# Performance work log

Hardware: AMD Instinct MI355X
Metric: run time of the kernel (lower is better)

The kernel has to match this reference:

```python
import jax, jax.numpy as jnp
import numpy as np
import math

NUM_HEADS = 16
KEY_SIZE = 64
HIDDEN = 4096
EMBED = 1024
VOCAB = 32000
SEQ = 2048
LAYERS = 4


def rmsnorm(x):
    return x * jax.lax.rsqrt(jnp.mean(x * x, axis=-1, keepdims=True) + 1e-5)


def rope_buffers(seq, d):
    half = d // 2
    i = jnp.arange(d)
    offset = i % half
    scales = jnp.power(10000.0, (-2.0 / d) * offset.astype(jnp.float32))
    m = jnp.arange(seq, dtype=jnp.float32)
    angles = m[:, None] * scales[None, :]  # [S, D]
    cos = jnp.cos(angles)
    sin = jnp.sin(angles)
    sin = jnp.concatenate([-sin[:, :half], sin[:, half:]], axis=-1)
    return cos, sin


def rotate(x, cos, sin):
    # x: [B, H, S, D]; cos/sin: [S, D]
    half = KEY_SIZE // 2
    swapped = jnp.concatenate([x[..., half:], x[..., :half]], axis=-1)
    return cos[None, None] * x + sin[None, None] * swapped


def setup_inputs() -> dict:
    key = jax.random.key(0)
    ks = jax.random.split(key, 7)
    std = 0.02
    return {
        'tokens': jax.random.randint(ks[0], (1, SEQ), 0, VOCAB),
        'table': jax.random.normal(ks[1], (VOCAB, EMBED), jnp.float32) * std,
        'qkv_w': jax.random.normal(ks[2], (LAYERS, EMBED, 3 * NUM_HEADS * KEY_SIZE), jnp.float32) * std,
        'out_w': jax.random.normal(ks[3], (LAYERS, NUM_HEADS * KEY_SIZE, EMBED), jnp.float32) * std,
        'up_w': jax.random.normal(ks[4], (LAYERS, EMBED, 2 * HIDDEN), jnp.float32) * std,
        'down_w': jax.random.normal(ks[5], (LAYERS, HIDDEN, EMBED), jnp.float32) * std,
        'vocab_w': jax.random.normal(ks[6], (EMBED, VOCAB), jnp.float32) * std,
    }


def reference(tokens, table, qkv_w, out_w, up_w, down_w, vocab_w):
    B, S = tokens.shape
    H, D = NUM_HEADS, KEY_SIZE
    # module zeroes embedding row 0 each forward
    table = table.at[0].set(0.0)
    cos, sin = rope_buffers(S, D)
    causal = jnp.tril(jnp.ones((S, S), dtype=bool))  # context_size == S -> pure causal
    emb = table[tokens]  # [B, S, E]
    for l in range(LAYERS):
        # --- self attention ---
        normed = rmsnorm(emb)
        qkv = normed @ qkv_w[l]  # [B, S, 3HD]
        q, k, v = jnp.split(qkv, 3, axis=-1)
        q = q.reshape(B, S, H, D).transpose(0, 2, 1, 3)
        k = k.reshape(B, S, H, D).transpose(0, 2, 1, 3)
        v = v.reshape(B, S, H, D).transpose(0, 2, 1, 3)
        q = rotate(q, cos, sin)
        k = rotate(k, cos, sin)
        attn = jnp.einsum('bhqd,bhkd->bhqk', q, k) / math.sqrt(D)
        attn = jnp.where(causal[None, None], attn, -jnp.inf)
        attn = jax.nn.softmax(attn, axis=-1)
        out = jnp.einsum('bhqk,bhkd->bhqd', attn, v)
        out = out.transpose(0, 2, 1, 3).reshape(B, S, H * D)
        emb = emb + out @ out_w[l]
        # --- SwiGLU FFN ---
        normed = rmsnorm(emb)
        gate_up = normed @ up_w[l]
        gate, up = gate_up[..., :HIDDEN], gate_up[..., HIDDEN:]
        emb = emb + (up * jax.nn.silu(gate)) @ down_w[l]
    emb = rmsnorm(emb)
    logits = emb @ vocab_w  # [B, S, V]
    return logits
```

## Files before the change

### kernel.cpp

```cpp
#include <hip/hip_runtime.h>
#include <hip/hip_bf16.h>

typedef __attribute__((ext_vector_type(8))) short short8;
typedef __attribute__((ext_vector_type(4))) float f32x4;

__device__ __forceinline__ ushort f2bf(float f) {
  uint32_t u = __float_as_uint(f);
  uint32_t r = (u + 0x7FFFu + ((u >> 16) & 1u)) >> 16;
  return (ushort)r;
}
__device__ __forceinline__ float bf2f(ushort u) {
  return __uint_as_float(((uint32_t)u) << 16);
}

__device__ __forceinline__ void gload_lds16(const ushort* g, ushort* l) {
  __builtin_amdgcn_global_load_lds(
      (const __attribute__((address_space(1))) void*)g,
      (__attribute__((address_space(3))) void*)l, 16, 0, 0);
}

__device__ __forceinline__ f32x4 mfma16(short8 a, short8 b, f32x4 c) {
  return __builtin_amdgcn_mfma_f32_16x16x32_bf16(a, b, c, 0, 0, 0);
}

#define BAR() __builtin_amdgcn_s_barrier()
#define WAIT_LGKM()                                        \
  do {                                                     \
    asm volatile("s_waitcnt lgkmcnt(0)" ::: "memory");     \
    __builtin_amdgcn_sched_barrier(0);                     \
  } while (0)
#define WAIT_VM()                                          \
  do {                                                     \
    asm volatile("s_waitcnt vmcnt(0)" ::: "memory");       \
    __builtin_amdgcn_sched_barrier(0);                     \
  } while (0)

__global__ __launch_bounds__(256)
void transpose_conv_kernel(const float* __restrict__ W, ushort* __restrict__ WT,
                           const int K, const int N) {
  __shared__ float tile[32][33];
  const int n0 = blockIdx.x * 32;
  const int k0 = blockIdx.y * 32;
  const int x = threadIdx.x;
  const int y = threadIdx.y;
#pragma unroll
  for (int j = 0; j < 4; ++j)
    tile[y + j * 8][x] = W[(size_t)(k0 + y + j * 8) * N + n0 + x];
  __syncthreads();
#pragma unroll
  for (int j = 0; j < 4; ++j)
    WT[(size_t)(n0 + y + j * 8) * K + k0 + x] = f2bf(tile[x][y + j * 8]);
}

__global__ __launch_bounds__(256)
void embed_kernel(const int* __restrict__ tokens, const float* __restrict__ table,
                  float* __restrict__ emb) {
  const int s = blockIdx.x, t = threadIdx.x;
  const int tok = tokens[s];
  float4 v = make_float4(0.f, 0.f, 0.f, 0.f);
  if (tok != 0) v = *(const float4*)&table[(size_t)tok * 1024 + t * 4];
  *(float4*)&emb[(size_t)s * 1024 + t * 4] = v;
}

__global__ __launch_bounds__(256)
void rmsnorm_kernel(const float* __restrict__ x, ushort* __restrict__ out) {
  const int row = blockIdx.x, t = threadIdx.x;
  const float4 v = *(const float4*)&x[(size_t)row * 1024 + t * 4];
  float ss = v.x * v.x + v.y * v.y + v.z * v.z + v.w * v.w;
#pragma unroll
  for (int off = 32; off; off >>= 1) ss += __shfl_xor(ss, off);
  __shared__ float red[4];
  if ((t & 63) == 0) red[t >> 6] = ss;
  __syncthreads();
  const float total = red[0] + red[1] + red[2] + red[3];
  const float sc = rsqrtf(total * (1.f / 1024.f) + 1e-5f);
  ushort4 o;
  o.x = f2bf(v.x * sc); o.y = f2bf(v.y * sc);
  o.z = f2bf(v.z * sc); o.w = f2bf(v.w * sc);
  *(ushort4*)&out[(size_t)row * 1024 + t * 4] = o;
}

__global__ __launch_bounds__(256)
void rope_kernel(const float* __restrict__ qkv, ushort* __restrict__ qh,
                 ushort* __restrict__ kh) {
  const int s = blockIdx.x;
  const int t = threadIdx.x;
  const int e0 = t * 4;
  const int hh = e0 >> 6;
  const int d0 = e0 & 63;
  const float* row = qkv + (size_t)s * 3072;
  const int part = hh * 64 + ((d0 + 32) & 63);
  const float4 xq  = *(const float4*)&row[e0];
  const float4 xqs = *(const float4*)&row[part];
  const float4 xk  = *(const float4*)&row[1024 + e0];
  const float4 xks = *(const float4*)&row[1024 + part];
  float co[4], si[4];
#pragma unroll
  for (int c = 0; c < 4; ++c) {
    const int d = d0 + c;
    const int off = d & 31;
    const float freq = exp2f(-0.41524101186092029f * (float)off);
    const float ang = (float)s * freq;
    co[c] = cosf(ang);
    const float sv = sinf(ang);
    si[c] = (d < 32) ? -sv : sv;
  }
  ushort4 oq, ok;
  oq.x = f2bf(co[0] * xq.x + si[0] * xqs.x);
  oq.y = f2bf(co[1] * xq.y + si[1] * xqs.y);
  oq.z = f2bf(co[2] * xq.z + si[2] * xqs.z);
  oq.w = f2bf(co[3] * xq.w + si[3] * xqs.w);
  ok.x = f2bf(co[0] * xk.x + si[0] * xks.x);
  ok.y = f2bf(co[1] * xk.y + si[1] * xks.y);
  ok.z = f2bf(co[2] * xk.z + si[2] * xks.z);
  ok.w = f2bf(co[3] * xk.w + si[3] * xks.w);
  const size_t ho = ((size_t)hh * 2048 + s) * 64 + d0;
  *(ushort4*)&qh[ho] = oq;
  *(ushort4*)&kh[ho] = ok;
}

__global__ __launch_bounds__(256)
void vtrans_kernel(const float* __restrict__ qkvbuf, ushort* __restrict__ vt) {
  __shared__ float t[64][65];
  const int h = blockIdx.y;
  const int s0 = blockIdx.x * 64;
  const int tid = threadIdx.x;
#pragma unroll
  for (int j = 0; j < 4; ++j) {
    const int e = j * 1024 + tid * 4;
    const int r = e >> 6, c = e & 63;
    *(float4*)&t[r][c] = *(const float4*)&qkvbuf[(size_t)(s0 + r) * 3072 + 2048 + h * 64 + c];
  }
  __syncthreads();
#pragma unroll
  for (int j = 0; j < 4; ++j) {
    const int e = j * 1024 + tid * 4;
    const int d = e >> 6, s = e & 63;
    ushort4 ov;
    ov.x = f2bf(t[s + 0][d]);
    ov.y = f2bf(t[s + 1][d]);
    ov.z = f2bf(t[s + 2][d]);
    ov.w = f2bf(t[s + 3][d]);
    *(ushort4*)&vt[((size_t)h * 64 + d) * 2048 + s0 + s] = ov;
  }
}

__global__ __launch_bounds__(256)
void attn_mfma_kernel(const ushort* __restrict__ qh, const ushort* __restrict__ kh,
                      const ushort* __restrict__ vt, ushort* __restrict__ attn_out) {
  __shared__ ushort sQ[64 * 64];
  __shared__ ushort sK[64 * 64];
  __shared__ ushort sV[64 * 64];
  __shared__ ushort sP[4][1024];
  const int h = blockIdx.y;
  const int bx = blockIdx.x;
  const int qt = (h < 8) ? bx : 31 - bx;
  const int i0 = qt * 64;
  const int tid = threadIdx.x;
  const int w = tid >> 6, lane = tid & 63;
  const int llo = lane & 15, lhi = lane >> 4;
  const int lr = lane >> 3, lc = lane & 7;
  const ushort* qg = qh + ((size_t)h * 2048 + i0) * 64;
  const ushort* kg = kh + (size_t)h * 2048 * 64;
  const ushort* vg = vt + (size_t)h * 64 * 2048;

#pragma unroll
  for (int j = 0; j < 2; ++j) {
    const int r0 = (w * 2 + j) * 8;
    const int row = r0 + lr;
    gload_lds16(qg + (size_t)row * 64 + ((lc ^ (row & 7)) * 8), &sQ[r0 * 64]);
  }
  __syncthreads();
  const int qrow = w * 16 + llo;
  const short8 qf0 = *(const short8*)&sQ[qrow * 64 + ((lhi ^ (qrow & 7)) * 8)];
  const short8 qf1 = *(const short8*)&sQ[qrow * 64 + (((4 + lhi) ^ (qrow & 7)) * 8)];

  float m = -1e30f, lsum = 0.f;
  f32x4 o[4] = {};
  const int nch = qt + 1;
  for (int cb = 0; cb < nch; ++cb) {
    const int kb = cb * 64;
    __syncthreads();
#pragma unroll
    for (int j = 0; j < 2; ++j) {
      const int r0 = (w * 2 + j) * 8;
      const int row = r0 + lr;
      gload_lds16(kg + (size_t)(kb + row) * 64 + ((lc ^ (row & 7)) * 8), &sK[r0 * 64]);
      gload_lds16(vg + (size_t)row * 2048 + kb + ((lc ^ (row & 7)) * 8), &sV[r0 * 64]);
    }
    __syncthreads();

    f32x4 st[4] = {};
#pragma unroll
    for (int ck = 0; ck < 2; ++ck) {
      const short8 qf = ck ? qf1 : qf0;
#pragma unroll
      for (int f = 0; f < 4; ++f) {
        const int key = f * 16 + llo;
        const short8 kf = *(const short8*)&sK[key * 64 + (((ck * 4 + lhi) ^ (key & 7)) * 8)];
        st[f] = mfma16(kf, qf, st[f]);
      }
    }

    float pv[4][4];
    const bool diag = (kb == i0);
#pragma unroll
    for (int f = 0; f < 4; ++f)
#pragma unroll
      for (int r = 0; r < 4; ++r) {
        float x = st[f][r] * 0.125f;
        if (diag && (f * 16 + lhi * 4 + r) > qrow) x = -1e30f;
        pv[f][r] = x;
      }
    float mr = pv[0][0];
#pragma unroll
    for (int f = 0; f < 4; ++f)
#pragma unroll
      for (int r = 0; r < 4; ++r) mr = fmaxf(mr, pv[f][r]);
    mr = fmaxf(mr, __shfl_xor(mr, 16));
    mr = fmaxf(mr, __shfl_xor(mr, 32));
    const float mnew = fmaxf(m, mr);
    const float scale = __expf(m - mnew);
    m = mnew;
    float rs = 0.f;
#pragma unroll
    for (int f = 0; f < 4; ++f)
#pragma unroll
      for (int r = 0; r < 4; ++r) {
        const float p = __expf(pv[f][r] - mnew);
        pv[f][r] = p;
        rs += p;
      }
    rs += __shfl_xor(rs, 16);
    rs += __shfl_xor(rs, 32);
    lsum = lsum * scale + rs;
    float scr[4];
#pragma unroll
    for (int r = 0; r < 4; ++r) scr[r] = __shfl(scale, lhi * 4 + r);
#pragma unroll
    for (int nn = 0; nn < 4; ++nn)
#pragma unroll
      for (int r = 0; r < 4; ++r) o[nn][r] *= scr[r];

    ushort* pw = sP[w];
#pragma unroll
    for (int f = 0; f < 4; ++f) {
      uint2 pk;
      pk.x = (uint)f2bf(pv[f][0]) | ((uint)f2bf(pv[f][1]) << 16);
      pk.y = (uint)f2bf(pv[f][2]) | ((uint)f2bf(pv[f][3]) << 16);
      *(uint2*)&pw[llo * 64 + ((f * 16 + lhi * 4) ^ ((llo & 7) << 3))] = pk;
    }
    const short8 pf0 = *(const short8*)&pw[llo * 64 + ((lhi ^ (llo & 7)) * 8)];
    const short8 pf1 = *(const short8*)&pw[llo * 64 + (((4 + lhi) ^ (llo & 7)) * 8)];

#pragma unroll
    for (int ck = 0; ck < 2; ++ck) {
      const short8 pf = ck ? pf1 : pf0;
#pragma unroll
      for (int nn = 0; nn < 4; ++nn) {
        const int drow = nn * 16 + llo;
        const short8 vf = *(const short8*)&sV[drow * 64 + (((ck * 4 + lhi) ^ (drow & 7)) * 8)];
        o[nn] = mfma16(pf, vf, o[nn]);
      }
    }
  }

  const float inv = 1.f / lsum;
  float invr[4];
#pragma unroll
  for (int r = 0; r < 4; ++r) invr[r] = __shfl(inv, lhi * 4 + r);
#pragma unroll
  for (int nn = 0; nn < 4; ++nn)
#pragma unroll
    for (int r = 0; r < 4; ++r) {
      const int row = i0 + w * 16 + lhi * 4 + r;
      attn_out[(size_t)row * 1024 + h * 64 + nn * 16 + llo] = f2bf(o[nn][r] * invr[r]);
    }
}

__global__ __launch_bounds__(256)
void silu_mul_kernel(const ushort* __restrict__ gu, ushort* __restrict__ hb) {
  const int idx = blockIdx.x * 256 + threadIdx.x;
  const int i = idx * 4;
  const int r = i >> 12;
  const int c = i & 4095;
  const ushort4 g4 = *(const ushort4*)&gu[(size_t)r * 8192 + c];
  const ushort4 u4 = *(const ushort4*)&gu[(size_t)r * 8192 + 4096 + c];
  ushort4 o;
  {
    float gv = bf2f(g4.x), uv = bf2f(u4.x);
    o.x = f2bf(uv * gv / (1.f + expf(-gv)));
  }
  {
    float gv = bf2f(g4.y), uv = bf2f(u4.y);
    o.y = f2bf(uv * gv / (1.f + expf(-gv)));
  }
  {
    float gv = bf2f(g4.z), uv = bf2f(u4.z);
    o.z = f2bf(uv * gv / (1.f + expf(-gv)));
  }
  {
    float gv = bf2f(g4.w), uv = bf2f(u4.w);
    o.w = f2bf(uv * gv / (1.f + expf(-gv)));
  }
  *(ushort4*)&hb[(size_t)r * 4096 + c] = o;
}

template <int BM, int BN, int EPI>
__global__ __launch_bounds__(256)
void gemm_bt_kernel(const ushort* __restrict__ A, const ushort* __restrict__ BT,
                    const float* __restrict__ addend, void* __restrict__ Cout,
                    const int M, const int N, const int K) {
  constexpr int WM = BM / 2, WN = BN / 2;
  constexpr int FM = WM / 16, FN = WN / 16;
  constexpr int CHA = BM / 16, CHB = BN / 16;
  __shared__ ushort sA[BM * 32];
  __shared__ ushort sB[BN * 32];
  const int bm0 = blockIdx.y * BM;
  const int bn0 = blockIdx.x * BN;
  const int tid = threadIdx.x;
  const int wid = tid >> 6;
  const int lane = tid & 63;
  const int wr = wid >> 1, wc = wid & 1;
  const int lhi = lane >> 4, llo = lane & 15;
  f32x4 acc[FM][FN] = {};
  for (int kt = 0; kt < K; kt += 32) {
#pragma unroll
    for (int c2 = 0; c2 < CHA / 4; ++c2) {
      const int ch = c2 * 4 + wid;
      const int e = ch * 512 + lane * 8;
      gload_lds16(A + (size_t)(bm0 + (e >> 5)) * K + kt + (e & 31), sA + ch * 512);
    }
#pragma unroll
    for (int c2 = 0; c2 < CHB / 4; ++c2) {
      const int ch = c2 * 4 + wid;
      const int e = ch * 512 + lane * 8;
      gload_lds16(BT + (size_t)(bn0 + (e >> 5)) * K + kt + (e & 31), sB + ch * 512);
    }
    __syncthreads();
    short8 aF[FM], bF[FN];
#pragma unroll
    for (int mm = 0; mm < FM; ++mm)
      aF[mm] = *(const short8*)&sA[(wr * WM + mm * 16 + llo) * 32 + lhi * 8];
#pragma unroll
    for (int nn = 0; nn < FN; ++nn)
      bF[nn] = *(const short8*)&sB[(wc * WN + nn * 16 + llo) * 32 + lhi * 8];
#pragma unroll
    for (int mm = 0; mm < FM; ++mm)
#pragma unroll
      for (int nn = 0; nn < FN; ++nn)
        acc[mm][nn] = __builtin_amdgcn_mfma_f32_16x16x32_bf16(aF[mm], bF[nn],
                                                              acc[mm][nn], 0, 0, 0);
    __syncthreads();
  }
#pragma unroll
  for (int mm = 0; mm < FM; ++mm) {
#pragma unroll
    for (int nn = 0; nn < FN; ++nn) {
      const int col = bn0 + wc * WN + nn * 16 + llo;
#pragma unroll
      for (int r = 0; r < 4; ++r) {
        const int row = bm0 + wr * WM + mm * 16 + lhi * 4 + r;
        float v = acc[mm][nn][r];
        if constexpr (EPI == 2) {
          ((ushort*)Cout)[(size_t)row * N + col] = f2bf(v);
        } else {
          if constexpr (EPI == 1) v += addend[(size_t)row * N + col];
          ((float*)Cout)[(size_t)row * N + col] = v;
        }
      }
    }
  }
}

#define LDA_(MH)                                                              \
  {                                                                           \
    _Pragma("unroll") for (int mm = 0; mm < 4; ++mm) {                        \
      const int row = wr * 128 + ((MH) * 4 + mm) * 16 + llo;                  \
      _Pragma("unroll") for (int ks = 0; ks < 2; ++ks)                        \
          aF[mm][ks] = *(const short8*)&cA[row * 64 +                         \
                          (((ks * 4 + lhi) ^ (row & 7)) * 8)];                \
    }                                                                         \
  }
#define LDB_(NH)                                                              \
  {                                                                           \
    _Pragma("unroll") for (int nn = 0; nn < 2; ++nn) {                        \
      const int row = wc * 64 + ((NH) * 2 + nn) * 16 + llo;                   \
      _Pragma("unroll") for (int ks = 0; ks < 2; ++ks)                        \
          bF[nn][ks] = *(const short8*)&cB[row * 64 +                         \
                          (((ks * 4 + lhi) ^ (row & 7)) * 8)];                \
    }                                                                         \
  }
#define MFMAQ_(MH, NH)                                                        \
  {                                                                           \
    __builtin_amdgcn_s_setprio(1);                                            \
    _Pragma("unroll") for (int mm = 0; mm < 4; ++mm)                          \
        _Pragma("unroll") for (int nn = 0; nn < 2; ++nn)                      \
            _Pragma("unroll") for (int ks = 0; ks < 2; ++ks)                  \
                acc[(MH) * 4 + mm][(NH) * 2 + nn] =                           \
                    mfma16(aF[mm][ks], bF[nn][ks],                            \
                           acc[(MH) * 4 + mm][(NH) * 2 + nn]);                \
    __builtin_amdgcn_s_setprio(0);                                            \
  }

template <int EPI>
__global__ __launch_bounds__(512, 2)
void gemm8_kernel(const ushort* __restrict__ A, const ushort* __restrict__ BT,
                  const float* __restrict__ addend, void* __restrict__ Cout,
                  const int M, const int N, const int K, const int nbx) {
  extern __shared__ ushort smem[];
  const int nwg = gridDim.x;
  const int cpx = nwg >> 3;
  int id = blockIdx.x;
  id = (id & 7) * cpx + (id >> 3);
  const int bx = id % nbx, by = id / nbx;
  const int bm0 = by * 256, bn0 = bx * 256;
  const int tid = threadIdx.x;
  const int wid = tid >> 6, lane = tid & 63;
  const int wr = wid >> 2, wc = wid & 3;
  const int llo = lane & 15, lhi = lane >> 4;
  const ushort* gA = A + (size_t)bm0 * K;
  const ushort* gB = BT + (size_t)bn0 * K;

  auto stage = [&](const ushort* g, ushort* dst, int kt) {
#pragma unroll
    for (int i = 0; i < 4; ++i) {
      const int chunk = i * 512 + wid * 64 + lane;
      const int row = chunk >> 3, c = chunk & 7;
      gload_lds16(g + (size_t)row * K + kt + ((c ^ (row & 7)) * 8),
                  dst + (size_t)(i * 512 + wid * 64) * 8);
    }
  };

  f32x4 acc[8][4] = {};
  short8 aF[4][2];
  short8 bF[2][2];

  stage(gA, smem, 0);
  stage(gB, smem + 16384, 0);
  WAIT_VM();
  BAR();

  const int nt = K >> 6;
  for (int t = 0; t < nt; ++t) {
    const int cur = t & 1;
    ushort* cA = smem + cur * 32768;
    ushort* cB = cA + 16384;
    ushort* nA = smem + (cur ^ 1) * 32768;
    ushort* nB = nA + 16384;
    const bool pf = (t + 1 < nt);
    LDA_(0); LDB_(0);
    if (pf) { stage(gA, nA, (t + 1) * 64); stage(gB, nB, (t + 1) * 64); }
    BAR(); WAIT_LGKM();
    MFMAQ_(0, 0);
    BAR();
    LDB_(1);
    BAR(); WAIT_LGKM();
    MFMAQ_(0, 1);
    BAR();
    LDA_(1);
    BAR(); WAIT_LGKM();
    MFMAQ_(1, 1);
    BAR();
    LDB_(0);
    BAR(); WAIT_LGKM();
    MFMAQ_(1, 0);
    if (pf) WAIT_VM();
    BAR();
  }

#pragma unroll
  for (int m = 0; m < 8; ++m) {
#pragma unroll
    for (int n = 0; n < 4; ++n) {
      const int col = bn0 + wc * 64 + n * 16 + llo;
#pragma unroll
      for (int r = 0; r < 4; ++r) {
        const int row = bm0 + wr * 128 + m * 16 + lhi * 4 + r;
        float v = acc[m][n][r];
        if constexpr (EPI == 2) {
          ((ushort*)Cout)[(size_t)row * N + col] = f2bf(v);
        } else {
          if constexpr (EPI == 1) v += addend[(size_t)row * N + col];
          ((float*)Cout)[(size_t)row * N + col] = v;
        }
      }
    }
  }
}

extern "C" void kernel_launch(void* const* d_in, const int* in_sizes, int n_in,
                              void* d_out, int out_size, void* d_ws, size_t ws_size,
                              hipStream_t stream) {
  const int* tokens    = (const int*)d_in[0];
  const float* table   = (const float*)d_in[1];
  const float* qkv_w   = (const float*)d_in[2];
  const float* out_w   = (const float*)d_in[3];
  const float* up_w    = (const float*)d_in[4];
  const float* down_w  = (const float*)d_in[5];
  const float* vocab_w = (const float*)d_in[6];
  float* logits = (float*)d_out;

  constexpr int G8_LDS = 131072;
  hipFuncSetAttribute(reinterpret_cast<const void*>(&gemm8_kernel<0>),
                      hipFuncAttributeMaxDynamicSharedMemorySize, G8_LDS);
  hipFuncSetAttribute(reinterpret_cast<const void*>(&gemm8_kernel<2>),
                      hipFuncAttributeMaxDynamicSharedMemorySize, G8_LDS);

  char* p = (char*)d_ws;
  auto alloc = [&](size_t bytes) {
    char* r = p;
    p += (bytes + 255) & ~(size_t)255;
    return r;
  };
  float*  emb    = (float*)alloc(2048ull * 1024 * 4);
  ushort* normed = (ushort*)alloc(2048ull * 1024 * 2);
  float*  qkvbuf = (float*)alloc(2048ull * 3072 * 4);
  ushort* qhb    = (ushort*)alloc(16ull * 2048 * 64 * 2);
  ushort* khb    = (ushort*)alloc(16ull * 2048 * 64 * 2);
  ushort* vtb    = (ushort*)alloc(16ull * 64 * 2048 * 2);
  ushort* attno  = (ushort*)alloc(2048ull * 1024 * 2);
  ushort* gateup = (ushort*)alloc(2048ull * 8192 * 2);
  ushort* hbuf   = (ushort*)alloc(2048ull * 4096 * 2);
  ushort* qkvT   = (ushort*)alloc(4ull * 3072 * 1024 * 2);
  ushort* outT   = (ushort*)alloc(4ull * 1024 * 1024 * 2);
  ushort* upT    = (ushort*)alloc(4ull * 8192 * 1024 * 2);
  ushort* downT  = (ushort*)alloc(4ull * 1024 * 4096 * 2);
  ushort* vocabT = (ushort*)alloc(32000ull * 1024 * 2);

  const dim3 tb(32, 8);
  for (int l = 0; l < 4; ++l) {
    transpose_conv_kernel<<<dim3(3072 / 32, 1024 / 32), tb, 0, stream>>>(
        qkv_w + (size_t)l * 1024 * 3072, qkvT + (size_t)l * 3072 * 1024, 1024, 3072);
    transpose_conv_kernel<<<dim3(1024 / 32, 1024 / 32), tb, 0, stream>>>(
        out_w + (size_t)l * 1024 * 1024, outT + (size_t)l * 1024 * 1024, 1024, 1024);
    transpose_conv_kernel<<<dim3(8192 / 32, 1024 / 32), tb, 0, stream>>>(
        up_w + (size_t)l * 1024 * 8192, upT + (size_t)l * 8192 * 1024, 1024, 8192);
    transpose_conv_kernel<<<dim3(1024 / 32, 4096 / 32), tb, 0, stream>>>(
        down_w + (size_t)l * 4096 * 1024, downT + (size_t)l * 1024 * 4096, 4096, 1024);
  }
  transpose_conv_kernel<<<dim3(32000 / 32, 1024 / 32), tb, 0, stream>>>(
      vocab_w, vocabT, 1024, 32000);

  embed_kernel<<<2048, 256, 0, stream>>>(tokens, table, emb);

  for (int l = 0; l < 4; ++l) {
    rmsnorm_kernel<<<2048, 256, 0, stream>>>(emb, normed);
    gemm8_kernel<0><<<(3072 / 256) * (2048 / 256), 512, G8_LDS, stream>>>(
        normed, qkvT + (size_t)l * 3072 * 1024, nullptr, qkvbuf,
        2048, 3072, 1024, 3072 / 256);
    rope_kernel<<<2048, 256, 0, stream>>>(qkvbuf, qhb, khb);
    vtrans_kernel<<<dim3(32, 16), 256, 0, stream>>>(qkvbuf, vtb);
    attn_mfma_kernel<<<dim3(32, 16), 256, 0, stream>>>(qhb, khb, vtb, attno);
    gemm_bt_kernel<64, 128, 1><<<dim3(1024 / 128, 2048 / 64), 256, 0, stream>>>(
        attno, outT + (size_t)l * 1024 * 1024, emb, emb, 2048, 1024, 1024);
    rmsnorm_kernel<<<2048, 256, 0, stream>>>(emb, normed);
    gemm8_kernel<2><<<(8192 / 256) * (2048 / 256), 512, G8_LDS, stream>>>(
        normed, upT + (size_t)l * 8192 * 1024, nullptr, gateup,
        2048, 8192, 1024, 8192 / 256);
    silu_mul_kernel<<<8192, 256, 0, stream>>>(gateup, hbuf);
    gemm_bt_kernel<64, 128, 1><<<dim3(1024 / 128, 2048 / 64), 256, 0, stream>>>(
        hbuf, downT + (size_t)l * 1024 * 4096, emb, emb, 2048, 1024, 4096);
  }
  rmsnorm_kernel<<<2048, 256, 0, stream>>>(emb, normed);
  gemm8_kernel<0><<<(32000 / 256) * (2048 / 256), 512, G8_LDS, stream>>>(
      normed, vocabT, nullptr, logits, 2048, 32000, 1024, 32000 / 256);
}
```

Measured before the change: 1.384 ms.

## Fuse SiLU into up-proj GEMM, merge rope/vtrans, retile residual GEMMs

The up-projection weight rows are interleaved so gate and up columns land in adjacent lanes. SwiGLU is then computed in the gemm8 epilogue with a shuffle, which removes the gateup buffer and the separate silu kernel. The rope and V-transpose kernels are merged into one launch, the residual GEMMs move from 64x128 to 128x128 tiles, and the vocab logits use nontemporal stores. The cost is a shuffle-based epilogue in which half the lanes store, and fewer blocks for the residual GEMMs.

```diff
diff --git a/kernel.cpp b/kernel.cpp
--- a/kernel.cpp
+++ b/kernel.cpp
@@ -37,7 +37,7 @@
 
 __global__ __launch_bounds__(256)
 void transpose_conv_kernel(const float* __restrict__ W, ushort* __restrict__ WT,
-                           const int K, const int N) {
+                           const int K, const int N, const int mode) {
   __shared__ float tile[32][33];
   const int n0 = blockIdx.x * 32;
   const int k0 = blockIdx.y * 32;
@@ -48,8 +48,11 @@
     tile[y + j * 8][x] = W[(size_t)(k0 + y + j * 8) * N + n0 + x];
   __syncthreads();
 #pragma unroll
-  for (int j = 0; j < 4; ++j)
-    WT[(size_t)(n0 + y + j * 8) * K + k0 + x] = f2bf(tile[x][y + j * 8]);
+  for (int j = 0; j < 4; ++j) {
+    int r = n0 + y + j * 8;
+    if (mode == 1) r = (r < 4096) ? (2 * r) : (2 * (r - 4096) + 1);
+    WT[(size_t)r * K + k0 + x] = f2bf(tile[x][y + j * 8]);
+  }
 }
 
 __global__ __launch_bounds__(256)
@@ -81,67 +84,59 @@
 }
 
 __global__ __launch_bounds__(256)
-void rope_kernel(const float* __restrict__ qkv, ushort* __restrict__ qh,
-                 ushort* __restrict__ kh) {
-  const int s = blockIdx.x;
-  const int t = threadIdx.x;
-  const int e0 = t * 4;
-  const int hh = e0 >> 6;
-  const int d0 = e0 & 63;
-  const float* row = qkv + (size_t)s * 3072;
-  const int part = hh * 64 + ((d0 + 32) & 63);
-  const float4 xq  = *(const float4*)&row[e0];
-  const float4 xqs = *(const float4*)&row[part];
-  const float4 xk  = *(const float4*)&row[1024 + e0];
-  const float4 xks = *(const float4*)&row[1024 + part];
-  float co[4], si[4];
-#pragma unroll
-  for (int c = 0; c < 4; ++c) {
-    const int d = d0 + c;
-    const int off = d & 31;
-    const float freq = exp2f(-0.41524101186092029f * (float)off);
-    const float ang = (float)s * freq;
-    co[c] = cosf(ang);
-    const float sv = sinf(ang);
-    si[c] = (d < 32) ? -sv : sv;
-  }
-  ushort4 oq, ok;
-  oq.x = f2bf(co[0] * xq.x + si[0] * xqs.x);
-  oq.y = f2bf(co[1] * xq.y + si[1] * xqs.y);
-  oq.z = f2bf(co[2] * xq.z + si[2] * xqs.z);
-  oq.w = f2bf(co[3] * xq.w + si[3] * xqs.w);
-  ok.x = f2bf(co[0] * xk.x + si[0] * xks.x);
-  ok.y = f2bf(co[1] * xk.y + si[1] * xks.y);
-  ok.z = f2bf(co[2] * xk.z + si[2] * xks.z);
-  ok.w = f2bf(co[3] * xk.w + si[3] * xks.w);
-  const size_t ho = ((size_t)hh * 2048 + s) * 64 + d0;
-  *(ushort4*)&qh[ho] = oq;
-  *(ushort4*)&kh[ho] = ok;
-}
-
-__global__ __launch_bounds__(256)
-void vtrans_kernel(const float* __restrict__ qkvbuf, ushort* __restrict__ vt) {
-  __shared__ float t[64][65];
+void ropev_kernel(const float* __restrict__ qkv, ushort* __restrict__ qh,
+                  ushort* __restrict__ kh, ushort* __restrict__ vt) {
+  __shared__ float tv[64][65];
   const int h = blockIdx.y;
   const int s0 = blockIdx.x * 64;
-  const int tid = threadIdx.x;
+  const int t = threadIdx.x;
 #pragma unroll
   for (int j = 0; j < 4; ++j) {
-    const int e = j * 1024 + tid * 4;
-    const int r = e >> 6, c = e & 63;
-    *(float4*)&t[r][c] = *(const float4*)&qkvbuf[(size_t)(s0 + r) * 3072 + 2048 + h * 64 + c];
+    const int e = j * 1024 + t * 4;
+    const int sl = e >> 6, d0 = e & 63;
+    const int s = s0 + sl;
+    const float* row = qkv + (size_t)s * 3072 + h * 64;
+    const float4 xq  = *(const float4*)&row[d0];
+    const float4 xqs = *(const float4*)&row[(d0 + 32) & 63];
+    const float4 xk  = *(const float4*)&row[1024 + d0];
+    const float4 xks = *(const float4*)&row[1024 + ((d0 + 32) & 63)];
+    const float4 xv  = *(const float4*)&row[2048 + d0];
+    float co[4], si[4];
+#pragma unroll
+    for (int c = 0; c < 4; ++c) {
+      const int d = d0 + c;
+      const int off = d & 31;
+      const float freq = exp2f(-0.41524101186092029f * (float)off);
+      const float ang = (float)s * freq;
+      co[c] = cosf(ang);
+      const float sv = sinf(ang);
+      si[c] = (d < 32) ? -sv : sv;
+    }
+    ushort4 oq, ok;
+    oq.x = f2bf(co[0] * xq.x + si[0] * xqs.x);
+    oq.y = f2bf(co[1] * xq.y + si[1] * xqs.y);
+    oq.z = f2bf(co[2] * xq.z + si[2] * xqs.z);
+    oq.w = f2bf(co[3] * xq.w + si[3] * xqs.w);
+    ok.x = f2bf(co[0] * xk.x + si[0] * xks.x);
+    ok.y = f2bf(co[1] * xk.y + si[1] * xks.y);
+    ok.z = f2bf(co[2] * xk.z + si[2] * xks.z);
+    ok.w = f2bf(co[3] * xk.w + si[3] * xks.w);
+    const size_t ho = ((size_t)h * 2048 + s) * 64 + d0;
+    *(ushort4*)&qh[ho] = oq;
+    *(ushort4*)&kh[ho] = ok;
+    *(float4*)&tv[sl][d0] = xv;
   }
   __syncthreads();
 #pragma unroll
   for (int j = 0; j < 4; ++j) {
-    const int e = j * 1024 + tid * 4;
-    const int d = e >> 6, s = e & 63;
+    const int e = j * 1024 + t * 4;
+    const int d = e >> 6, s4 = e & 63;
     ushort4 ov;
-    ov.x = f2bf(t[s + 0][d]);
-    ov.y = f2bf(t[s + 1][d]);
-    ov.z = f2bf(t[s + 2][d]);
-    ov.w = f2bf(t[s + 3][d]);
-    *(ushort4*)&vt[((size_t)h * 64 + d) * 2048 + s0 + s] = ov;
+    ov.x = f2bf(tv[s4 + 0][d]);
+    ov.y = f2bf(tv[s4 + 1][d]);
+    ov.z = f2bf(tv[s4 + 2][d]);
+    ov.w = f2bf(tv[s4 + 3][d]);
+    *(ushort4*)&vt[((size_t)h * 64 + d) * 2048 + s0 + s4] = ov;
   }
 }
 
@@ -276,34 +271,6 @@
       const int row = i0 + w * 16 + lhi * 4 + r;
       attn_out[(size_t)row * 1024 + h * 64 + nn * 16 + llo] = f2bf(o[nn][r] * invr[r]);
     }
-}
-
-__global__ __launch_bounds__(256)
-void silu_mul_kernel(const ushort* __restrict__ gu, ushort* __restrict__ hb) {
-  const int idx = blockIdx.x * 256 + threadIdx.x;
-  const int i = idx * 4;
-  const int r = i >> 12;
-  const int c = i & 4095;
-  const ushort4 g4 = *(const ushort4*)&gu[(size_t)r * 8192 + c];
-  const ushort4 u4 = *(const ushort4*)&gu[(size_t)r * 8192 + 4096 + c];
-  ushort4 o;
-  {
-    float gv = bf2f(g4.x), uv = bf2f(u4.x);
-    o.x = f2bf(uv * gv / (1.f + expf(-gv)));
-  }
-  {
-    float gv = bf2f(g4.y), uv = bf2f(u4.y);
-    o.y = f2bf(uv * gv / (1.f + expf(-gv)));
-  }
-  {
-    float gv = bf2f(g4.z), uv = bf2f(u4.z);
-    o.z = f2bf(uv * gv / (1.f + expf(-gv)));
-  }
-  {
-    float gv = bf2f(g4.w), uv = bf2f(u4.w);
-    o.w = f2bf(uv * gv / (1.f + expf(-gv)));
-  }
-  *(ushort4*)&hb[(size_t)r * 4096 + c] = o;
 }
 
 template <int BM, int BN, int EPI>
@@ -478,10 +445,16 @@
       for (int r = 0; r < 4; ++r) {
         const int row = bm0 + wr * 128 + m * 16 + lhi * 4 + r;
         float v = acc[m][n][r];
-        if constexpr (EPI == 2) {
-          ((ushort*)Cout)[(size_t)row * N + col] = f2bf(v);
+        if constexpr (EPI == 3) {
+          const float other = __shfl_xor(v, 1);
+          if ((llo & 1) == 0) {
+            const float gate = v, up = other;
+            const float hh = up * gate / (1.f + expf(-gate));
+            ((ushort*)Cout)[(size_t)row * (N >> 1) + (col >> 1)] = f2bf(hh);
+          }
+        } else if constexpr (EPI == 4) {
+          __builtin_nontemporal_store(v, &((float*)Cout)[(size_t)row * N + col]);
         } else {
-          if constexpr (EPI == 1) v += addend[(size_t)row * N + col];
           ((float*)Cout)[(size_t)row * N + col] = v;
         }
       }
@@ -504,7 +477,9 @@
   constexpr int G8_LDS = 131072;
   hipFuncSetAttribute(reinterpret_cast<const void*>(&gemm8_kernel<0>),
                       hipFuncAttributeMaxDynamicSharedMemorySize, G8_LDS);
-  hipFuncSetAttribute(reinterpret_cast<const void*>(&gemm8_kernel<2>),
+  hipFuncSetAttribute(reinterpret_cast<const void*>(&gemm8_kernel<3>),
+                      hipFuncAttributeMaxDynamicSharedMemorySize, G8_LDS);
+  hipFuncSetAttribute(reinterpret_cast<const void*>(&gemm8_kernel<4>),
                       hipFuncAttributeMaxDynamicSharedMemorySize, G8_LDS);
 
   char* p = (char*)d_ws;
@@ -520,7 +495,6 @@
   ushort* khb    = (ushort*)alloc(16ull * 2048 * 64 * 2);
   ushort* vtb    = (ushort*)alloc(16ull * 64 * 2048 * 2);
   ushort* attno  = (ushort*)alloc(2048ull * 1024 * 2);
-  ushort* gateup = (ushort*)alloc(2048ull * 8192 * 2);
   ushort* hbuf   = (ushort*)alloc(2048ull * 4096 * 2);
   ushort* qkvT   = (ushort*)alloc(4ull * 3072 * 1024 * 2);
   ushort* outT   = (ushort*)alloc(4ull * 1024 * 1024 * 2);
@@ -531,16 +505,16 @@
   const dim3 tb(32, 8);
   for (int l = 0; l < 4; ++l) {
     transpose_conv_kernel<<<dim3(3072 / 32, 1024 / 32), tb, 0, stream>>>(
-        qkv_w + (size_t)l * 1024 * 3072, qkvT + (size_t)l * 3072 * 1024, 1024, 3072);
+        qkv_w + (size_t)l * 1024 * 3072, qkvT + (size_t)l * 3072 * 1024, 1024, 3072, 0);
     transpose_conv_kernel<<<dim3(1024 / 32, 1024 / 32), tb, 0, stream>>>(
-        out_w + (size_t)l * 1024 * 1024, outT + (size_t)l * 1024 * 1024, 1024, 1024);
+        out_w + (size_t)l * 1024 * 1024, outT + (size_t)l * 1024 * 1024, 1024, 1024, 0);
     transpose_conv_kernel<<<dim3(8192 / 32, 1024 / 32), tb, 0, stream>>>(
-        up_w + (size_t)l * 1024 * 8192, upT + (size_t)l * 8192 * 1024, 1024, 8192);
+        up_w + (size_t)l * 1024 * 8192, upT + (size_t)l * 8192 * 1024, 1024, 8192, 1);
     transpose_conv_kernel<<<dim3(1024 / 32, 4096 / 32), tb, 0, stream>>>(
-        down_w + (size_t)l * 4096 * 1024, downT + (size_t)l * 1024 * 4096, 4096, 1024);
+        down_w + (size_t)l * 4096 * 1024, downT + (size_t)l * 1024 * 4096, 4096, 1024, 0);
   }
   transpose_conv_kernel<<<dim3(32000 / 32, 1024 / 32), tb, 0, stream>>>(
-      vocab_w, vocabT, 1024, 32000);
+      vocab_w, vocabT, 1024, 32000, 0);
 
   embed_kernel<<<2048, 256, 0, stream>>>(tokens, table, emb);
 
@@ -549,20 +523,18 @@
     gemm8_kernel<0><<<(3072 / 256) * (2048 / 256), 512, G8_LDS, stream>>>(
         normed, qkvT + (size_t)l * 3072 * 1024, nullptr, qkvbuf,
         2048, 3072, 1024, 3072 / 256);
-    rope_kernel<<<2048, 256, 0, stream>>>(qkvbuf, qhb, khb);
-    vtrans_kernel<<<dim3(32, 16), 256, 0, stream>>>(qkvbuf, vtb);
+    ropev_kernel<<<dim3(32, 16), 256, 0, stream>>>(qkvbuf, qhb, khb, vtb);
     attn_mfma_kernel<<<dim3(32, 16), 256, 0, stream>>>(qhb, khb, vtb, attno);
-    gemm_bt_kernel<64, 128, 1><<<dim3(1024 / 128, 2048 / 64), 256, 0, stream>>>(
+    gemm_bt_kernel<128, 128, 1><<<dim3(1024 / 128, 2048 / 128), 256, 0, stream>>>(
         attno, outT + (size_t)l * 1024 * 1024, emb, emb, 2048, 1024, 1024);
     rmsnorm_kernel<<<2048, 256, 0, stream>>>(emb, normed);
-    gemm8_kernel<2><<<(8192 / 256) * (2048 / 256), 512, G8_LDS, stream>>>(
-        normed, upT + (size_t)l * 8192 * 1024, nullptr, gateup,
+    gemm8_kernel<3><<<(8192 / 256) * (2048 / 256), 512, G8_LDS, stream>>>(
+        normed, upT + (size_t)l * 8192 * 1024, nullptr, hbuf,
         2048, 8192, 1024, 8192 / 256);
-    silu_mul_kernel<<<8192, 256, 0, stream>>>(gateup, hbuf);
-    gemm_bt_kernel<64, 128, 1><<<dim3(1024 / 128, 2048 / 64), 256, 0, stream>>>(
+    gemm_bt_kernel<128, 128, 1><<<dim3(1024 / 128, 2048 / 128), 256, 0, stream>>>(
         hbuf, downT + (size_t)l * 1024 * 4096, emb, emb, 2048, 1024, 4096);
   }
   rmsnorm_kernel<<<2048, 256, 0, stream>>>(emb, normed);
-  gemm8_kernel<0><<<(32000 / 256) * (2048 / 256), 512, G8_LDS, stream>>>(
+  gemm8_kernel<4><<<(32000 / 256) * (2048 / 256), 512, G8_LDS, stream>>>(
       normed, vocabT, nullptr, logits, 2048, 32000, 1024, 32000 / 256);
 }
```

Result: slower. 1.509 ms (+9.0%).
